# Kernel optimization log

Hardware: AMD Instinct MI355X
Metric: run time of the kernel (lower is better)

The kernel has to match this reference:

```python
import jax, jax.numpy as jnp
import numpy as np

WS = 14          # window size
NH = 12          # num heads
C = 768          # hidden dim
HD = C // NH     # head dim = 64
MLP = 3072       # mlp dim
EPS = 1e-6


def _layernorm(x, g, b):
    mu = jnp.mean(x, axis=-1, keepdims=True)
    var = jnp.mean(jnp.square(x - mu), axis=-1, keepdims=True)
    return (x - mu) * jax.lax.rsqrt(var + EPS) * g + b


def setup_inputs() -> dict:
    key = jax.random.key(0)
    ks = jax.random.split(key, 8)
    B, H, W = 8, 64, 64
    f32 = jnp.float32
    d = {}
    d["x"] = jax.random.normal(ks[0], (B, H, W, C), f32)
    d["ln1_g"] = jnp.ones((C,), f32)
    d["ln1_b"] = jnp.zeros((C,), f32)
    d["qkv_w"] = (jax.random.normal(ks[1], (C, 3 * C), f32) * 0.02)
    d["qkv_b"] = jnp.zeros((3 * C,), f32)
    d["proj_w"] = (jax.random.normal(ks[2], (C, C), f32) * 0.02)
    d["proj_b"] = jnp.zeros((C,), f32)
    d["rel_pos_h"] = (jax.random.normal(ks[3], (2 * WS - 1, HD), f32) * 0.02)
    d["rel_pos_w"] = (jax.random.normal(ks[4], (2 * WS - 1, HD), f32) * 0.02)
    d["ln2_g"] = jnp.ones((C,), f32)
    d["ln2_b"] = jnp.zeros((C,), f32)
    d["mlp_w1"] = (jax.random.normal(ks[5], (C, MLP), f32) * 0.02)
    d["mlp_b1"] = jnp.zeros((MLP,), f32)
    d["mlp_w2"] = (jax.random.normal(ks[6], (MLP, C), f32) * 0.02)
    d["mlp_b2"] = jnp.zeros((C,), f32)
    return d


def reference(x, ln1_g, ln1_b, qkv_w, qkv_b, proj_w, proj_b,
              rel_pos_h, rel_pos_w, ln2_g, ln2_b,
              mlp_w1, mlp_b1, mlp_w2, mlp_b2):
    B, H, W, _ = x.shape
    xn = _layernorm(x, ln1_g, ln1_b)

    # ---- window partition (pad to multiple of WS) ----
    pad_h = (-H) % WS
    pad_w = (-W) % WS
    Hp, Wp = H + pad_h, W + pad_w
    xp = jnp.pad(xn, ((0, 0), (0, pad_h), (0, pad_w), (0, 0)))
    # [B, Hp/WS, WS, Wp/WS, WS, C] -> [Bn, WS, WS, C]
    win = xp.reshape(B, Hp // WS, WS, Wp // WS, WS, C)
    win = win.transpose(0, 1, 3, 2, 4, 5).reshape(-1, WS, WS, C)
    Bn = win.shape[0]
    N = WS * WS

    # ---- attention with decomposed relative position bias ----
    qkv = win.reshape(Bn, N, C) @ qkv_w + qkv_b                 # [Bn, N, 3C]
    qkv = qkv.reshape(Bn, N, 3, NH, HD).transpose(2, 0, 3, 1, 4)
    qkv = qkv.reshape(3, Bn * NH, N, HD)
    q, k, v = qkv[0], qkv[1], qkv[2]

    scale = HD ** -0.5
    attn = jnp.einsum('bnd,bmd->bnm', q * scale, k)             # [Bn*NH, N, N]

    # rel coords: q_size == k_size == WS, rel_pos already has 2*WS-1 rows
    coords = jnp.arange(WS)[:, None] - jnp.arange(WS)[None, :] + (WS - 1)
    Rh = rel_pos_h[coords]                                      # [WS, WS, HD]
    Rw = rel_pos_w[coords]                                      # [WS, WS, HD]
    rq = q.reshape(Bn * NH, WS, WS, HD)
    rel_h = jnp.einsum('bhwc,hkc->bhwk', rq, Rh)                # [B', WS, WS, WS]
    rel_w = jnp.einsum('bhwc,wkc->bhwk', rq, Rw)
    attn = (attn.reshape(Bn * NH, WS, WS, WS, WS)
            + rel_h[:, :, :, :, None]
            + rel_w[:, :, :, None, :]).reshape(Bn * NH, N, N)

    attn = jax.nn.softmax(attn, axis=-1)
    out = jnp.einsum('bnm,bmd->bnd', attn, v)                   # [Bn*NH, N, HD]
    out = out.reshape(Bn, NH, WS, WS, HD).transpose(0, 2, 3, 1, 4).reshape(Bn, WS, WS, C)
    out = out @ proj_w + proj_b

    # ---- window unpartition ----
    out = out.reshape(B, Hp // WS, Wp // WS, WS, WS, C)
    out = out.transpose(0, 1, 3, 2, 4, 5).reshape(B, Hp, Wp, C)[:, :H, :W, :]

    x1 = x + out
    y = _layernorm(x1, ln2_g, ln2_b)
    y = jax.nn.gelu(y @ mlp_w1 + mlp_b1, approximate=False) @ mlp_w2 + mlp_b2
    return x1 + y
```

## Files before the change

### kernel.cpp

```cpp
#include <hip/hip_runtime.h>
#include <hip/hip_bf16.h>
#include <cstdint>
#include <cstddef>

using bf16 = __hip_bfloat16;
typedef __attribute__((ext_vector_type(8))) short short8;
typedef __attribute__((ext_vector_type(4))) float f32x4;

typedef __attribute__((address_space(1))) const void as1_void;
typedef __attribute__((address_space(3))) void as3_void;

__device__ __forceinline__ f32x4 mfma16x16x32(short8 a, short8 b, f32x4 c) {
  return __builtin_amdgcn_mfma_f32_16x16x32_bf16(a, b, c, 0, 0, 0);
}

__device__ __forceinline__ void gload_lds16(const void* g, void* l) {
  __builtin_amdgcn_global_load_lds((as1_void*)g, (as3_void*)l, 16, 0, 0);
}

__device__ __forceinline__ uint32_t cvtpk(float a, float b) {
  uint32_t r;
  asm("v_cvt_pk_bf16_f32 %0, %1, %2" : "=v"(r) : "v"(a), "v"(b));
  return r;
}

__device__ __forceinline__ float gelu_f(float v) {
  const float u = 0.7978845608f * v * (1.f + 0.044715f * v * v);
  const float e = __expf(-2.f * fabsf(u));
  const float t = (1.f - e) / (1.f + e);
  return 0.5f * v * (1.f + (u < 0.f ? -t : t));
}

static constexpr int MROWS = 39200;
static constexpr int MPAD  = 39424;
static constexpr int TOK2  = 32768;

__global__ __launch_bounds__(256)
void transpose_cast(const float* __restrict__ in, bf16* __restrict__ out, int K, int N) {
  __shared__ float t[32][33];
  const int tx = threadIdx.x & 31, ty = threadIdx.x >> 5;
  const int bx = blockIdx.x, by = blockIdx.y;
  const int x = bx * 32 + tx;
  for (int r = ty; r < 32; r += 8)
    t[r][tx] = in[(size_t)(by * 32 + r) * N + x];
  __syncthreads();
  const int xo = by * 32 + tx;
  for (int r = ty; r < 32; r += 8)
    out[(size_t)(bx * 32 + r) * K + xo] = __float2bfloat16(t[tx][r]);
}

__global__ __launch_bounds__(256)
void ln1_partition(const float* __restrict__ x, const float* __restrict__ g,
                   const float* __restrict__ bb, bf16* __restrict__ out) {
  const int token = blockIdx.x * 4 + (threadIdx.x >> 6);
  const int lane = threadIdx.x & 63;
  const int win = token / 196, tok = token % 196;
  const int b_ = win / 25, wh = (win / 5) % 5, ww = win % 5;
  const int i = tok / 14, j = tok % 14;
  const int h = wh * 14 + i, w = ww * 14 + j;
  bf16* o = out + (size_t)token * 768;
  if (h >= 64 || w >= 64) {
    for (int t = 0; t < 12; ++t) o[lane + 64 * t] = __float2bfloat16(0.f);
    return;
  }
  const float* src = x + ((size_t)((b_ * 64 + h) * 64 + w)) * 768;
  float vals[12], s = 0.f, ss = 0.f;
  #pragma unroll
  for (int t = 0; t < 12; ++t) {
    float v = src[lane + 64 * t];
    vals[t] = v; s += v; ss += v * v;
  }
  #pragma unroll
  for (int d = 32; d > 0; d >>= 1) { s += __shfl_xor(s, d); ss += __shfl_xor(ss, d); }
  const float mu = s * (1.f / 768.f);
  const float var = ss * (1.f / 768.f) - mu * mu;
  const float inv = rsqrtf(var + 1e-6f);
  #pragma unroll
  for (int t = 0; t < 12; ++t) {
    const int c = lane + 64 * t;
    o[c] = __float2bfloat16((vals[t] - mu) * inv * g[c] + bb[c]);
  }
}

__global__ __launch_bounds__(256)
void ln2_kernel(const float* __restrict__ x1, const float* __restrict__ g,
                const float* __restrict__ bb, bf16* __restrict__ out) {
  const int token = blockIdx.x * 4 + (threadIdx.x >> 6);
  const int lane = threadIdx.x & 63;
  const float* src = x1 + (size_t)token * 768;
  bf16* o = out + (size_t)token * 768;
  float vals[12], s = 0.f, ss = 0.f;
  #pragma unroll
  for (int t = 0; t < 12; ++t) {
    float v = src[lane + 64 * t];
    vals[t] = v; s += v; ss += v * v;
  }
  #pragma unroll
  for (int d = 32; d > 0; d >>= 1) { s += __shfl_xor(s, d); ss += __shfl_xor(ss, d); }
  const float mu = s * (1.f / 768.f);
  const float var = ss * (1.f / 768.f) - mu * mu;
  const float inv = rsqrtf(var + 1e-6f);
  #pragma unroll
  for (int t = 0; t < 12; ++t) {
    const int c = lane + 64 * t;
    o[c] = __float2bfloat16((vals[t] - mu) * inv * g[c] + bb[c]);
  }
}

template<int EPI>
__global__ __launch_bounds__(256)
void gemm_bf16(const bf16* __restrict__ A, const bf16* __restrict__ Bt,
               const float* __restrict__ bias, int K, int Mreal,
               const float* __restrict__ fin, float* __restrict__ fout,
               bf16* __restrict__ ob0, bf16* __restrict__ ob1, bf16* __restrict__ ob2) {
  __shared__ __align__(16) bf16 SMEM[16384];
  bf16* const lA0 = SMEM;
  bf16* const lA1 = SMEM + 4096;
  bf16* const lB0 = SMEM + 8192;
  bf16* const lB1 = SMEM + 12288;
  const int tid = threadIdx.x;
  const int lane = tid & 63, wv = tid >> 6;
  const int lr = lane & 15, hi = lane >> 4;
  const int wm = wv >> 1, wn = wv & 1;

  const int gx = gridDim.x;
  const int nwg = gx * gridDim.y;
  int lin = blockIdx.y * gx + blockIdx.x;
  {
    const int q8 = nwg >> 3, r8 = nwg & 7;
    const int xcd = lin & 7, pos = lin >> 3;
    lin = (xcd < r8 ? xcd * (q8 + 1) : r8 * (q8 + 1) + (xcd - r8) * q8) + pos;
  }
  const size_t arow0 = (size_t)(lin / gx) * 128;
  const size_t brow0 = (size_t)(lin % gx) * 128;
  f32x4 acc[4][4] = {};

  auto stage = [&](bf16* bufA, bf16* bufB, int kt) {
    const int k0 = kt * 32;
    #pragma unroll
    for (int it = 0; it < 2; ++it) {
      const int seg = it * 256 + tid;
      const int row = seg >> 2, kq = seg & 3;
      const size_t dst = (size_t)(it * 256 + wv * 64) * 8;
      if constexpr (EPI == 1) {
        const int k = k0 + kq * 8;
        gload_lds16(A + ((size_t)(k >> 6) * MPAD + arow0 + row) * 64 + (k & 63), bufA + dst);
      } else {
        gload_lds16(A + (arow0 + row) * K + k0 + kq * 8, bufA + dst);
      }
      gload_lds16(Bt + (brow0 + row) * K + k0 + kq * 8, bufB + dst);
    }
  };
  auto compute = [&](const bf16* bufA, const bf16* bufB) {
    short8 af[4], bfr[4];
    #pragma unroll
    for (int m = 0; m < 4; ++m) af[m] = *(const short8*)&bufA[(wm * 64 + m * 16 + lr) * 32 + hi * 8];
    #pragma unroll
    for (int n = 0; n < 4; ++n) bfr[n] = *(const short8*)&bufB[(wn * 64 + n * 16 + lr) * 32 + hi * 8];
    #pragma unroll
    for (int m = 0; m < 4; ++m)
      #pragma unroll
      for (int n = 0; n < 4; ++n)
        acc[m][n] = mfma16x16x32(af[m], bfr[n], acc[m][n]);
  };

  const int nt = K >> 5;
  stage(lA0, lB0, 0);
  __syncthreads();
  for (int t = 0; t < nt; t += 2) {
    if (t + 1 < nt) stage(lA1, lB1, t + 1);
    compute(lA0, lB0);
    __syncthreads();
    if (t + 2 < nt) stage(lA0, lB0, t + 2);
    compute(lA1, lB1);
    __syncthreads();
  }

  #pragma unroll
  for (int n = 0; n < 4; ++n) {
    const int col = (int)brow0 + wn * 64 + n * 16 + lr;
    const float bv = bias[col];
    #pragma unroll
    for (int m = 0; m < 4; ++m) {
      #pragma unroll
      for (int e = 0; e < 4; ++e) {
        const int row = (int)arow0 + wm * 64 + m * 16 + hi * 4 + e;
        const float v = acc[m][n][e] + bv;
        if (row < Mreal) {
          const int win = row / 196, tok = row % 196;
          const int b_ = win / 25, wh = (win / 5) % 5, ww = win % 5;
          const int i = tok / 14, j = tok % 14;
          const int h = wh * 14 + i, w = ww * 14 + j;
          if (h < 64 && w < 64) {
            const size_t idx = ((size_t)((b_ * 64 + h) * 64 + w)) * 768 + col;
            fout[idx] = fin[idx] + v;
          }
        }
      }
    }
  }
}

template<int MH, bool READB, int VMN>
__device__ __forceinline__ void gphase(
    const char* aR, const char* bR, int aoffB, int boffB,
    f32x4 (&acc)[8][4], short8& b0, short8& b1, short8& b2, short8& b3,
    const bf16* g0, const bf16* g1, char* sdst, int sdoff, int koff, bool doStage) {
  short8 a0 = *(const short8*)(aR + aoffB + (MH * 64 +  0) * 64);
  short8 a1 = *(const short8*)(aR + aoffB + (MH * 64 + 16) * 64);
  short8 a2 = *(const short8*)(aR + aoffB + (MH * 64 + 32) * 64);
  short8 a3 = *(const short8*)(aR + aoffB + (MH * 64 + 48) * 64);
  if constexpr (READB) {
    b0 = *(const short8*)(bR + boffB +  0 * 64);
    b1 = *(const short8*)(bR + boffB + 16 * 64);
    b2 = *(const short8*)(bR + boffB + 32 * 64);
    b3 = *(const short8*)(bR + boffB + 48 * 64);
  }
  if (doStage) {
    gload_lds16(g0 + koff, sdst + sdoff);
    gload_lds16(g1 + koff, sdst + sdoff + 8192);
  }
  __builtin_amdgcn_s_barrier();
  asm volatile("s_waitcnt lgkmcnt(0)" ::: "memory");
  __builtin_amdgcn_sched_barrier(0);
  __builtin_amdgcn_s_setprio(1);
  acc[MH*4+0][0] = mfma16x16x32(a0, b0, acc[MH*4+0][0]);
  acc[MH*4+0][1] = mfma16x16x32(a0, b1, acc[MH*4+0][1]);
  acc[MH*4+0][2] = mfma16x16x32(a0, b2, acc[MH*4+0][2]);
  acc[MH*4+0][3] = mfma16x16x32(a0, b3, acc[MH*4+0][3]);
  acc[MH*4+1][0] = mfma16x16x32(a1, b0, acc[MH*4+1][0]);
  acc[MH*4+1][1] = mfma16x16x32(a1, b1, acc[MH*4+1][1]);
  acc[MH*4+1][2] = mfma16x16x32(a1, b2, acc[MH*4+1][2]);
  acc[MH*4+1][3] = mfma16x16x32(a1, b3, acc[MH*4+1][3]);
  acc[MH*4+2][0] = mfma16x16x32(a2, b0, acc[MH*4+2][0]);
  acc[MH*4+2][1] = mfma16x16x32(a2, b1, acc[MH*4+2][1]);
  acc[MH*4+2][2] = mfma16x16x32(a2, b2, acc[MH*4+2][2]);
  acc[MH*4+2][3] = mfma16x16x32(a2, b3, acc[MH*4+2][3]);
  acc[MH*4+3][0] = mfma16x16x32(a3, b0, acc[MH*4+3][0]);
  acc[MH*4+3][1] = mfma16x16x32(a3, b1, acc[MH*4+3][1]);
  acc[MH*4+3][2] = mfma16x16x32(a3, b2, acc[MH*4+3][2]);
  acc[MH*4+3][3] = mfma16x16x32(a3, b3, acc[MH*4+3][3]);
  __builtin_amdgcn_s_setprio(0);
  if constexpr (VMN == 6) asm volatile("s_waitcnt vmcnt(6)" ::: "memory");
  if constexpr (VMN == 0) asm volatile("s_waitcnt vmcnt(0)" ::: "memory");
  __builtin_amdgcn_s_barrier();
}

template<int EPI, int KT>
__global__ __launch_bounds__(512)
void gemm256(const bf16* __restrict__ A, const bf16* __restrict__ Bt,
             const float* __restrict__ bias, int Mreal,
             const float* __restrict__ fin, float* __restrict__ fout,
             bf16* __restrict__ ob0, bf16* __restrict__ ob1, bf16* __restrict__ ob2) {
  __shared__ __align__(16) char SMEM[131072];
  char* const A0k0 = SMEM;
  char* const A0k1 = SMEM + 16384;
  char* const B0k0 = SMEM + 32768;
  char* const B0k1 = SMEM + 49152;
  char* const A1k0 = SMEM + 65536;
  char* const A1k1 = SMEM + 81920;
  char* const B1k0 = SMEM + 98304;
  char* const B1k1 = SMEM + 114688;
  const int tid = threadIdx.x;
  const int lane = tid & 63, wv = tid >> 6;
  const int lr = lane & 15, hi = lane >> 4;
  const int wm = wv >> 2, wn = wv & 3;

  const int gx = gridDim.x;
  const int nwg = gx * gridDim.y;
  int lin = blockIdx.y * gx + blockIdx.x;
  {
    const int q8 = nwg >> 3, r8 = nwg & 7;
    const int xcd = lin & 7, pos = lin >> 3;
    lin = (xcd < r8 ? xcd * (q8 + 1) : r8 * (q8 + 1) + (xcd - r8) * q8) + pos;
  }
  const size_t arow0 = (size_t)(lin / gx) * 256;
  const size_t brow0 = (size_t)(lin % gx) * 256;

  f32x4 acc[8][4] = {};
  short8 b0{}, b1{}, b2{}, b3{};
  constexpr int nt = KT >> 6;

  const int r0 = tid >> 2;
  const int c0 = (tid & 3) ^ ((r0 >> 1) & 3);
  const bf16* const gA0 = A  + (arow0 + r0) * (size_t)KT + c0 * 8;
  const bf16* const gA1 = gA0 + (size_t)128 * KT;
  const bf16* const gB0 = Bt + (brow0 + r0) * (size_t)KT + c0 * 8;
  const bf16* const gB1 = gB0 + (size_t)128 * KT;
  const int sdoff = tid << 4;
  const int cpos  = hi ^ ((lr >> 1) & 3);
  const int aoffB = (wm * 128 + lr) * 64 + (cpos << 4);
  const int boffB = (wn * 64 + lr) * 64 + (cpos << 4);

  auto stageU = [&](bool isB, int kt, int kh, char* dst) {
    if (kt >= nt) return;
    const int koff = (kt << 6) + (kh << 5);
    gload_lds16((isB ? gB0 : gA0) + koff, dst + sdoff);
    gload_lds16((isB ? gB1 : gA1) + koff, dst + sdoff + 8192);
  };

  stageU(true,  0, 0, B0k0);
  stageU(false, 0, 0, A0k0);
  stageU(true,  0, 1, B0k1);
  stageU(false, 0, 1, A0k1);
  stageU(true,  1, 0, B1k0);
  stageU(false, 1, 0, A1k0);
  stageU(true,  1, 1, B1k1);
  asm volatile("s_waitcnt vmcnt(6)" ::: "memory");
  __builtin_amdgcn_s_barrier();

  constexpr int niter = nt >> 1;
  for (int it = 0; it < niter - 1; ++it) {
    const int t = it * 2;
    const int kf1 = ((t+1) << 6) + 32, kf20 = (t+2) << 6, kf21 = kf20 + 32;
    const int kf30 = (t+3) << 6, kf31 = kf30 + 32;
    gphase<0,true ,-1>(A0k0, B0k0, aoffB, boffB, acc, b0,b1,b2,b3, gA0, gA1, A1k1, sdoff, kf1,  true);
    gphase<1,false,-1>(A0k0, B0k0, aoffB, boffB, acc, b0,b1,b2,b3, gB0, gB1, B0k0, sdoff, kf20, true);
    gphase<0,true ,-1>(A0k1, B0k1, aoffB, boffB, acc, b0,b1,b2,b3, gA0, gA1, A0k0, sdoff, kf20, true);
    gphase<1,false, 6>(A0k1, B0k1, aoffB, boffB, acc, b0,b1,b2,b3, gB0, gB1, B0k1, sdoff, kf21, true);
    gphase<0,true ,-1>(A1k0, B1k0, aoffB, boffB, acc, b0,b1,b2,b3, gA0, gA1, A0k1, sdoff, kf21, true);
    gphase<1,false,-1>(A1k0, B1k0, aoffB, boffB, acc, b0,b1,b2,b3, gB0, gB1, B1k0, sdoff, kf30, true);
    gphase<0,true ,-1>(A1k1, B1k1, aoffB, boffB, acc, b0,b1,b2,b3, gA0, gA1, A1k0, sdoff, kf30, true);
    gphase<1,false, 6>(A1k1, B1k1, aoffB, boffB, acc, b0,b1,b2,b3, gB0, gB1, B1k1, sdoff, kf31, true);
  }
  {
    const int t = nt - 2;
    const int kf1 = ((t+1) << 6) + 32;
    gphase<0,true ,-1>(A0k0, B0k0, aoffB, boffB, acc, b0,b1,b2,b3, gA0, gA1, A1k1, sdoff, kf1, true);
    gphase<1,false,-1>(A0k0, B0k0, aoffB, boffB, acc, b0,b1,b2,b3, gB0, gB1, B0k0, sdoff, 0, false);
    gphase<0,true ,-1>(A0k1, B0k1, aoffB, boffB, acc, b0,b1,b2,b3, gA0, gA1, A0k0, sdoff, 0, false);
    gphase<1,false, 0>(A0k1, B0k1, aoffB, boffB, acc, b0,b1,b2,b3, gB0, gB1, B0k1, sdoff, 0, false);
    gphase<0,true ,-1>(A1k0, B1k0, aoffB, boffB, acc, b0,b1,b2,b3, gA0, gA1, A0k1, sdoff, 0, false);
    gphase<1,false,-1>(A1k0, B1k0, aoffB, boffB, acc, b0,b1,b2,b3, gB0, gB1, B1k0, sdoff, 0, false);
    gphase<0,true ,-1>(A1k1, B1k1, aoffB, boffB, acc, b0,b1,b2,b3, gA0, gA1, A1k0, sdoff, 0, false);
    gphase<1,false, 0>(A1k1, B1k1, aoffB, boffB, acc, b0,b1,b2,b3, gB0, gB1, B1k1, sdoff, 0, false);
  }

  if constexpr (EPI == 0) {
    __syncthreads();
    char* ep = SMEM + wv * 16384;
    #pragma unroll
    for (int m = 0; m < 8; ++m) {
      #pragma unroll
      for (int n = 0; n < 4; ++n) {
        const int col = n * 16 + lr;
        const float bv = bias[(int)brow0 + wn * 64 + col];
        #pragma unroll
        for (int e = 0; e < 4; ++e) {
          const int row_l = m * 16 + hi * 4 + e;
          const int byte = row_l * 128 + col * 2;
          *(bf16*)(ep + (byte ^ ((row_l & 7) << 4))) = __float2bfloat16(acc[m][n][e] + bv);
        }
      }
    }
    __syncthreads();
    const int hchunk = ((int)brow0 + wn * 64) >> 6;
    const int which = hchunk / 12, head = hchunk % 12;
    bf16* dstb = (which == 0) ? ob0 : ((which == 1) ? ob1 : ob2);
    #pragma unroll
    for (int u = 0; u < 16; ++u) {
      const int unit = u * 64 + lane;
      const int row_l = unit >> 3, slot = unit & 7;
      const int byte = row_l * 128 + slot * 16;
      const short8 val = *(const short8*)(ep + (byte ^ ((row_l & 7) << 4)));
      const int grow = (int)arow0 + wm * 128 + row_l;
      if (grow < Mreal)
        *(short8*)&dstb[((size_t)head * MPAD + grow) * 64 + slot * 8] = val;
    }
  } else if constexpr (EPI == 2) {
    char* ep = SMEM + wv * 8192;
    #pragma unroll
    for (int h = 0; h < 2; ++h) {
      #pragma unroll
      for (int m2 = 0; m2 < 4; ++m2) {
        #pragma unroll
        for (int n = 0; n < 4; ++n) {
          const int col = n * 16 + lr;
          const float bv = bias[(int)brow0 + wn * 64 + col];
          #pragma unroll
          for (int e = 0; e < 4; ++e) {
            const int row_l = m2 * 16 + hi * 4 + e;
            const float v = gelu_f(acc[h * 4 + m2][n][e] + bv);
            *(bf16*)(ep + row_l * 128 + (((col >> 3) ^ (row_l & 7)) << 4) + ((col & 7) << 1))
                = __float2bfloat16(v);
          }
        }
      }
      #pragma unroll
      for (int p = 0; p < 8; ++p) {
        const int row_l = p * 8 + (lane >> 3);
        const int slot  = lane & 7;
        const short8 val = *(const short8*)(ep + row_l * 128 + ((slot ^ (row_l & 7)) << 4));
        const size_t grow = arow0 + wm * 128 + h * 64 + row_l;
        const int gcol = (int)brow0 + wn * 64 + slot * 8;
        *(short8*)&ob0[grow * 3072 + gcol] = val;
      }
    }
  } else {
    #pragma unroll
    for (int n = 0; n < 4; ++n) {
      const int col = (int)brow0 + wn * 64 + n * 16 + lr;
      const float bv = bias[col];
      #pragma unroll
      for (int m = 0; m < 8; ++m) {
        #pragma unroll
        for (int e = 0; e < 4; ++e) {
          const size_t row = arow0 + wm * 128 + m * 16 + hi * 4 + e;
          const size_t idx = row * 768 + col;
          fout[idx] = fin[idx] + acc[m][n][e] + bv;
        }
      }
    }
  }
}

__global__ __launch_bounds__(512, 2)
void attn_kernel(const bf16* __restrict__ qb, const bf16* __restrict__ kb,
                 const bf16* __restrict__ vb, const float* __restrict__ rph,
                 const float* __restrict__ rpw, bf16* __restrict__ aout) {
  __shared__ __align__(16) char SM[65248];
  bf16* pbh    = (bf16*)SM;
  bf16* pbw    = (bf16*)(SM + 4096);
  bf16* Gh     = (bf16*)(SM + 8192);
  bf16* Gw     = (bf16*)(SM + 23168);
  char* klds   = SM;
  char* vtb    = SM + 25600;
  bf16* relh_s = (bf16*)(SM + 54272);
  bf16* relw_s = (bf16*)(SM + 59760);

  const int bh = blockIdx.x;
  const int win = bh / 12, head = bh % 12;
  const size_t base = ((size_t)head * MPAD + win * 196) * 64;
  const bf16* Q  = qb + base;
  const bf16* Kp = kb + base;
  const bf16* Vp = vb + base;
  const int tid = threadIdx.x, lane = tid & 63, wv = tid >> 6;
  const int lr = lane & 15, hi = lane >> 4;

  for (int i = tid; i < 32 * 64; i += 512) {
    const int r = i >> 6, c = i & 63;
    const bool ok = r < 27;
    pbh[i] = __float2bfloat16(ok ? rph[r * 64 + c] : 0.f);
    pbw[i] = __float2bfloat16(ok ? rpw[r * 64 + c] : 0.f);
  }
  __syncthreads();
  {
    short8 bh00 = *(const short8*)&pbh[(lr) * 64 + hi * 8];
    short8 bh01 = *(const short8*)&pbh[(lr) * 64 + 32 + hi * 8];
    short8 bh10 = *(const short8*)&pbh[(16 + lr) * 64 + hi * 8];
    short8 bh11 = *(const short8*)&pbh[(16 + lr) * 64 + 32 + hi * 8];
    short8 bw00 = *(const short8*)&pbw[(lr) * 64 + hi * 8];
    short8 bw01 = *(const short8*)&pbw[(lr) * 64 + 32 + hi * 8];
    short8 bw10 = *(const short8*)&pbw[(16 + lr) * 64 + hi * 8];
    short8 bw11 = *(const short8*)&pbw[(16 + lr) * 64 + 32 + hi * 8];
    for (int mt = wv; mt < 13; mt += 8) {
      const short8 a0 = *(const short8*)&Q[(mt * 16 + lr) * 64 + hi * 8];
      const short8 a1 = *(const short8*)&Q[(mt * 16 + lr) * 64 + 32 + hi * 8];
      f32x4 g0 = {}, g1 = {}, g2 = {}, g3 = {};
      g0 = mfma16x16x32(a0, bh00, g0); g0 = mfma16x16x32(a1, bh01, g0);
      g1 = mfma16x16x32(a0, bh10, g1); g1 = mfma16x16x32(a1, bh11, g1);
      g2 = mfma16x16x32(a0, bw00, g2); g2 = mfma16x16x32(a1, bw01, g2);
      g3 = mfma16x16x32(a0, bw10, g3); g3 = mfma16x16x32(a1, bw11, g3);
      #pragma unroll
      for (int e = 0; e < 4; ++e) {
        const int row = mt * 16 + hi * 4 + e;
        Gh[row * 36 + lr]      = __float2bfloat16(g0[e]);
        Gh[row * 36 + 16 + lr] = __float2bfloat16(g1[e]);
        Gw[row * 36 + lr]      = __float2bfloat16(g2[e]);
        Gw[row * 36 + 16 + lr] = __float2bfloat16(g3[e]);
      }
    }
  }
  __syncthreads();
  bf16 ghr[6], gwr[6];
  #pragma unroll
  for (int t = 0; t < 6; ++t) {
    const int i = tid + t * 512;
    if (i < 196 * 14) {
      const int q = i / 14, kk = i - (i / 14) * 14;
      const int rh = q / 14 - kk + 13;
      const int rw2 = q - (q / 14) * 14 - kk + 13;
      ghr[t] = Gh[q * 36 + rh];
      gwr[t] = Gw[q * 36 + rw2];
    }
  }
  __syncthreads();
  #pragma unroll
  for (int t = 0; t < 6; ++t) {
    const int i = tid + t * 512;
    if (i < 196 * 14) { relh_s[i] = ghr[t]; relw_s[i] = gwr[t]; }
  }
  for (int c = wv; c < 25; c += 8) {
    const int row = c * 8 + (lane >> 3);
    const int ch  = (lane & 7) ^ (row & 7);
    gload_lds16(Kp + row * 64 + ch * 8, klds + c * 1024);
  }
  for (int i = tid; i < 196 * 8; i += 512) {
    const int key = i >> 3, dg = (i & 7) * 8;
    const short8 v = *(const short8*)&Vp[key * 64 + dg];
    #pragma unroll
    for (int j = 0; j < 8; ++j) {
      const int idx = (dg + j) * 448 + key * 2;
      *(bf16*)(vtb + (idx ^ (j << 4))) = ((const bf16*)&v)[j];
    }
  }
  for (int i = tid; i < 64 * 28; i += 512) {
    const int d = i / 28, key = 196 + i - (i / 28) * 28;
    const int idx = d * 448 + key * 2;
    *(bf16*)(vtb + (idx ^ ((d & 7) << 4))) = __float2bfloat16(0.f);
  }
  __syncthreads();

  for (int qt = wv; qt < 13; qt += 8) {
    const int q = qt * 16 + lr;
    const int qc = q < 196 ? q : 195;
    const short8 bq0 = *(const short8*)&Q[(qt * 16 + lr) * 64 + hi * 8];
    const short8 bq1 = *(const short8*)&Q[(qt * 16 + lr) * 64 + 32 + hi * 8];
    f32x4 s[13];
    __builtin_amdgcn_s_setprio(1);
    #pragma unroll
    for (int nt = 0; nt < 13; ++nt) {
      const int key = nt * 16 + lr;
      const char* kr = klds + key * 128;
      const short8 ka0 = *(const short8*)(kr + (((hi) ^ (key & 7)) << 4));
      const short8 ka1 = *(const short8*)(kr + (((hi + 4) ^ (key & 7)) << 4));
      f32x4 z = {};
      z = mfma16x16x32(ka0, bq0, z);
      z = mfma16x16x32(ka1, bq1, z);
      s[nt] = z;
    }
    __builtin_amdgcn_s_setprio(0);
    float mx = -3.0e38f;
    #pragma unroll
    for (int nt = 0; nt < 13; ++nt) {
      #pragma unroll
      for (int e = 0; e < 4; ++e) {
        const int key = nt * 16 + hi * 4 + e;
        const int kh = key / 14, kw = key - kh * 14;
        float v = s[nt][e] * 0.125f + __bfloat162float(relh_s[qc * 14 + kh])
                                    + __bfloat162float(relw_s[qc * 14 + kw]);
        v = (key < 196) ? v : -3.0e38f;
        s[nt][e] = v;
        mx = fmaxf(mx, v);
      }
    }
    mx = fmaxf(mx, __shfl_xor(mx, 16));
    mx = fmaxf(mx, __shfl_xor(mx, 32));
    float sm = 0.f;
    uint32_t pk0[14], pk1[14];
    #pragma unroll
    for (int nt = 0; nt < 13; ++nt) {
      const float p0 = __expf(s[nt][0] - mx);
      const float p1 = __expf(s[nt][1] - mx);
      const float p2 = __expf(s[nt][2] - mx);
      const float p3 = __expf(s[nt][3] - mx);
      sm += (p0 + p1) + (p2 + p3);
      pk0[nt] = cvtpk(p0, p1);
      pk1[nt] = cvtpk(p2, p3);
    }
    pk0[13] = 0u; pk1[13] = 0u;
    sm += __shfl_xor(sm, 16);
    sm += __shfl_xor(sm, 32);
    const float rinv = 1.f / sm;
    f32x4 o[4] = {};
    #pragma unroll
    for (int kk = 0; kk < 7; ++kk) {
      const uint32_t x0 = pk0[2 * kk],     x1 = pk1[2 * kk];
      const uint32_t y0 = pk0[2 * kk + 1], y1 = pk1[2 * kk + 1];
      const uint32_t s0 = (hi < 2) ? y0 : x0, s1 = (hi < 2) ? y1 : x1;
      const uint32_t t0 = __shfl_xor(s0, 32), t1 = __shfl_xor(s1, 32);
      const uint32_t o0 = (hi < 2) ? x0 : y0, o1 = (hi < 2) ? x1 : y1;
      const bool sendOwn = (hi == 1) || (hi == 2);
      const uint32_t u0 = sendOwn ? o0 : t0, u1 = sendOwn ? o1 : t1;
      const uint32_t r0 = __shfl_xor(u0, 16), r1 = __shfl_xor(u1, 16);
      union { uint32_t u[4]; short8 v; } pf;
      pf.u[0] = (hi == 0) ? x0 : ((hi == 2) ? t0 : r0);
      pf.u[1] = (hi == 0) ? x1 : ((hi == 2) ? t1 : r1);
      pf.u[2] = (hi == 3) ? y0 : ((hi == 1) ? t0 : r0);
      pf.u[3] = (hi == 3) ? y1 : ((hi == 1) ? t1 : r1);
      __builtin_amdgcn_s_setprio(1);
      #pragma unroll
      for (int n2 = 0; n2 < 4; ++n2) {
        const int d = n2 * 16 + lr;
        const int idx = d * 448 + (kk * 32 + hi * 8) * 2;
        const short8 va = *(const short8*)(vtb + (idx ^ ((lr & 7) << 4)));
        o[n2] = mfma16x16x32(va, pf.v, o[n2]);
      }
      __builtin_amdgcn_s_setprio(0);
    }
    if (q < 196) {
      bf16* orow = aout + ((size_t)head * MPAD + win * 196 + q) * 64;
      #pragma unroll
      for (int n2 = 0; n2 < 4; ++n2) {
        uint32_t d0 = cvtpk(o[n2][0] * rinv, o[n2][1] * rinv);
        uint32_t d1 = cvtpk(o[n2][2] * rinv, o[n2][3] * rinv);
        uint32_t* dst = (uint32_t*)&orow[n2 * 16 + hi * 4];
        dst[0] = d0; dst[1] = d1;
      }
    }
  }
}

extern "C" void kernel_launch(void* const* d_in, const int* in_sizes, int n_in,
                              void* d_out, int out_size, void* d_ws, size_t ws_size,
                              hipStream_t stream) {
  (void)in_sizes; (void)n_in; (void)out_size; (void)ws_size;
  const float* x      = (const float*)d_in[0];
  const float* ln1_g  = (const float*)d_in[1];
  const float* ln1_b  = (const float*)d_in[2];
  const float* qkv_w  = (const float*)d_in[3];
  const float* qkv_b  = (const float*)d_in[4];
  const float* proj_w = (const float*)d_in[5];
  const float* proj_b = (const float*)d_in[6];
  const float* rph    = (const float*)d_in[7];
  const float* rpw    = (const float*)d_in[8];
  const float* ln2_g  = (const float*)d_in[9];
  const float* ln2_b  = (const float*)d_in[10];
  const float* w1     = (const float*)d_in[11];
  const float* b1v    = (const float*)d_in[12];
  const float* w2     = (const float*)d_in[13];
  const float* b2v    = (const float*)d_in[14];
  float* outp = (float*)d_out;

  char* ws = (char*)d_ws;
  size_t off = 0;
  auto alloc = [&](size_t bytes) { char* p = ws + off; off += (bytes + 255) & ~(size_t)255; return p; };
  bf16* qkv_wt  = (bf16*)alloc((size_t)2304 * 768 * 2);
  bf16* proj_wt = (bf16*)alloc((size_t)768 * 768 * 2);
  bf16* w1t     = (bf16*)alloc((size_t)3072 * 768 * 2);
  bf16* w2t     = (bf16*)alloc((size_t)768 * 3072 * 2);
  const size_t szB1 = (size_t)MPAD * 768 * 2;
  const size_t szB2 = (size_t)TOK2 * 768 * 2;
  char* regB = alloc(szB1 > szB2 ? szB1 : szB2);
  const size_t szQKV = (size_t)3 * 12 * MPAD * 64 * 2;
  const size_t szH   = (size_t)TOK2 * 3072 * 2;
  char* regC = alloc(szQKV > szH ? szQKV : szH);

  bf16* xnwin   = (bf16*)regB;
  bf16* attnout = (bf16*)regB;
  bf16* xn2     = (bf16*)regB;
  bf16* qbuf    = (bf16*)regC;
  bf16* kbuf    = qbuf + (size_t)12 * MPAD * 64;
  bf16* vbuf    = kbuf + (size_t)12 * MPAD * 64;
  bf16* hbuf    = (bf16*)regC;

  transpose_cast<<<dim3(2304 / 32, 768 / 32), 256, 0, stream>>>(qkv_w, qkv_wt, 768, 2304);
  transpose_cast<<<dim3(768 / 32, 768 / 32), 256, 0, stream>>>(proj_w, proj_wt, 768, 768);
  transpose_cast<<<dim3(3072 / 32, 768 / 32), 256, 0, stream>>>(w1, w1t, 768, 3072);
  transpose_cast<<<dim3(768 / 32, 3072 / 32), 256, 0, stream>>>(w2, w2t, 3072, 768);

  ln1_partition<<<dim3(MROWS / 4), 256, 0, stream>>>(x, ln1_g, ln1_b, xnwin);

  gemm256<0, 768><<<dim3(2304 / 256, MPAD / 256), 512, 0, stream>>>(
      xnwin, qkv_wt, qkv_b, MROWS, nullptr, nullptr, qbuf, kbuf, vbuf);

  attn_kernel<<<dim3(2400), 512, 0, stream>>>(qbuf, kbuf, vbuf, rph, rpw, attnout);

  gemm_bf16<1><<<dim3(768 / 128, MPAD / 128), 256, 0, stream>>>(
      attnout, proj_wt, proj_b, 768, MROWS, x, outp, nullptr, nullptr, nullptr);

  ln2_kernel<<<dim3(TOK2 / 4), 256, 0, stream>>>(outp, ln2_g, ln2_b, xn2);

  gemm256<2, 768><<<dim3(3072 / 256, TOK2 / 256), 512, 0, stream>>>(
      xn2, w1t, b1v, TOK2, nullptr, nullptr, hbuf, nullptr, nullptr);
  gemm256<3, 3072><<<dim3(768 / 256, TOK2 / 256), 512, 0, stream>>>(
      hbuf, w2t, b2v, TOK2, outp, outp, nullptr, nullptr, nullptr);
}
```

Before: 1.042 ms.

## Shrink GEMM LDS pipeline to two-stage double buffer and split epilogue

Replaces the four-slot (two k-tiles by two k-halves) LDS staging in the 256x256 GEMM with a simple two-buffer ping-pong over 32-wide k steps. Each phase now waits for all outstanding loads before its barrier, so less memory latency is hidden. The QKV epilogue is also reworked to write through per-wave 8KB LDS tiles in two halves instead of 16KB tiles, which removes the extra syncthreads. LDS use halves to 64KB, which may permit more co-resident workgroups, at the cost of a shallower prefetch depth.

```diff
diff --git a/kernel.cpp b/kernel.cpp
--- a/kernel.cpp
+++ b/kernel.cpp
@@ -241,7 +241,6 @@
   acc[MH*4+3][2] = mfma16x16x32(a3, b2, acc[MH*4+3][2]);
   acc[MH*4+3][3] = mfma16x16x32(a3, b3, acc[MH*4+3][3]);
   __builtin_amdgcn_s_setprio(0);
-  if constexpr (VMN == 6) asm volatile("s_waitcnt vmcnt(6)" ::: "memory");
   if constexpr (VMN == 0) asm volatile("s_waitcnt vmcnt(0)" ::: "memory");
   __builtin_amdgcn_s_barrier();
 }
@@ -252,15 +251,11 @@
              const float* __restrict__ bias, int Mreal,
              const float* __restrict__ fin, float* __restrict__ fout,
              bf16* __restrict__ ob0, bf16* __restrict__ ob1, bf16* __restrict__ ob2) {
-  __shared__ __align__(16) char SMEM[131072];
-  char* const A0k0 = SMEM;
-  char* const A0k1 = SMEM + 16384;
-  char* const B0k0 = SMEM + 32768;
-  char* const B0k1 = SMEM + 49152;
-  char* const A1k0 = SMEM + 65536;
-  char* const A1k1 = SMEM + 81920;
-  char* const B1k0 = SMEM + 98304;
-  char* const B1k1 = SMEM + 114688;
+  __shared__ __align__(16) char SMEM[65536];
+  char* const A0 = SMEM;
+  char* const B0 = SMEM + 16384;
+  char* const A1 = SMEM + 32768;
+  char* const B1 = SMEM + 49152;
   const int tid = threadIdx.x;
   const int lane = tid & 63, wv = tid >> 6;
   const int lr = lane & 15, hi = lane >> 4;
@@ -279,7 +274,7 @@
 
   f32x4 acc[8][4] = {};
   short8 b0{}, b1{}, b2{}, b3{};
-  constexpr int nt = KT >> 6;
+  constexpr int nt = KT >> 5;
 
   const int r0 = tid >> 2;
   const int c0 = (tid & 3) ^ ((r0 >> 1) & 3);
@@ -292,80 +287,52 @@
   const int aoffB = (wm * 128 + lr) * 64 + (cpos << 4);
   const int boffB = (wn * 64 + lr) * 64 + (cpos << 4);
 
-  auto stageU = [&](bool isB, int kt, int kh, char* dst) {
-    if (kt >= nt) return;
-    const int koff = (kt << 6) + (kh << 5);
-    gload_lds16((isB ? gB0 : gA0) + koff, dst + sdoff);
-    gload_lds16((isB ? gB1 : gA1) + koff, dst + sdoff + 8192);
-  };
-
-  stageU(true,  0, 0, B0k0);
-  stageU(false, 0, 0, A0k0);
-  stageU(true,  0, 1, B0k1);
-  stageU(false, 0, 1, A0k1);
-  stageU(true,  1, 0, B1k0);
-  stageU(false, 1, 0, A1k0);
-  stageU(true,  1, 1, B1k1);
-  asm volatile("s_waitcnt vmcnt(6)" ::: "memory");
+  gload_lds16(gA0, A0 + sdoff);
+  gload_lds16(gA1, A0 + sdoff + 8192);
+  gload_lds16(gB0, B0 + sdoff);
+  gload_lds16(gB1, B0 + sdoff + 8192);
+  asm volatile("s_waitcnt vmcnt(0)" ::: "memory");
   __builtin_amdgcn_s_barrier();
 
-  constexpr int niter = nt >> 1;
-  for (int it = 0; it < niter - 1; ++it) {
-    const int t = it * 2;
-    const int kf1 = ((t+1) << 6) + 32, kf20 = (t+2) << 6, kf21 = kf20 + 32;
-    const int kf30 = (t+3) << 6, kf31 = kf30 + 32;
-    gphase<0,true ,-1>(A0k0, B0k0, aoffB, boffB, acc, b0,b1,b2,b3, gA0, gA1, A1k1, sdoff, kf1,  true);
-    gphase<1,false,-1>(A0k0, B0k0, aoffB, boffB, acc, b0,b1,b2,b3, gB0, gB1, B0k0, sdoff, kf20, true);
-    gphase<0,true ,-1>(A0k1, B0k1, aoffB, boffB, acc, b0,b1,b2,b3, gA0, gA1, A0k0, sdoff, kf20, true);
-    gphase<1,false, 6>(A0k1, B0k1, aoffB, boffB, acc, b0,b1,b2,b3, gB0, gB1, B0k1, sdoff, kf21, true);
-    gphase<0,true ,-1>(A1k0, B1k0, aoffB, boffB, acc, b0,b1,b2,b3, gA0, gA1, A0k1, sdoff, kf21, true);
-    gphase<1,false,-1>(A1k0, B1k0, aoffB, boffB, acc, b0,b1,b2,b3, gB0, gB1, B1k0, sdoff, kf30, true);
-    gphase<0,true ,-1>(A1k1, B1k1, aoffB, boffB, acc, b0,b1,b2,b3, gA0, gA1, A1k0, sdoff, kf30, true);
-    gphase<1,false, 6>(A1k1, B1k1, aoffB, boffB, acc, b0,b1,b2,b3, gB0, gB1, B1k1, sdoff, kf31, true);
-  }
-  {
-    const int t = nt - 2;
-    const int kf1 = ((t+1) << 6) + 32;
-    gphase<0,true ,-1>(A0k0, B0k0, aoffB, boffB, acc, b0,b1,b2,b3, gA0, gA1, A1k1, sdoff, kf1, true);
-    gphase<1,false,-1>(A0k0, B0k0, aoffB, boffB, acc, b0,b1,b2,b3, gB0, gB1, B0k0, sdoff, 0, false);
-    gphase<0,true ,-1>(A0k1, B0k1, aoffB, boffB, acc, b0,b1,b2,b3, gA0, gA1, A0k0, sdoff, 0, false);
-    gphase<1,false, 0>(A0k1, B0k1, aoffB, boffB, acc, b0,b1,b2,b3, gB0, gB1, B0k1, sdoff, 0, false);
-    gphase<0,true ,-1>(A1k0, B1k0, aoffB, boffB, acc, b0,b1,b2,b3, gA0, gA1, A0k1, sdoff, 0, false);
-    gphase<1,false,-1>(A1k0, B1k0, aoffB, boffB, acc, b0,b1,b2,b3, gB0, gB1, B1k0, sdoff, 0, false);
-    gphase<0,true ,-1>(A1k1, B1k1, aoffB, boffB, acc, b0,b1,b2,b3, gA0, gA1, A1k0, sdoff, 0, false);
-    gphase<1,false, 0>(A1k1, B1k1, aoffB, boffB, acc, b0,b1,b2,b3, gB0, gB1, B1k1, sdoff, 0, false);
+  for (int t = 0; t < nt; t += 2) {
+    const int k1 = (t + 1) << 5, k2 = (t + 2) << 5;
+    const bool s1 = (t + 1) < nt, s2 = (t + 2) < nt;
+    gphase<0,true ,-1>(A0, B0, aoffB, boffB, acc, b0,b1,b2,b3, gA0, gA1, A1, sdoff, k1, s1);
+    gphase<1,false, 0>(A0, B0, aoffB, boffB, acc, b0,b1,b2,b3, gB0, gB1, B1, sdoff, k1, s1);
+    gphase<0,true ,-1>(A1, B1, aoffB, boffB, acc, b0,b1,b2,b3, gA0, gA1, A0, sdoff, k2, s2);
+    gphase<1,false, 0>(A1, B1, aoffB, boffB, acc, b0,b1,b2,b3, gB0, gB1, B0, sdoff, k2, s2);
   }
 
   if constexpr (EPI == 0) {
-    __syncthreads();
-    char* ep = SMEM + wv * 16384;
-    #pragma unroll
-    for (int m = 0; m < 8; ++m) {
-      #pragma unroll
-      for (int n = 0; n < 4; ++n) {
-        const int col = n * 16 + lr;
-        const float bv = bias[(int)brow0 + wn * 64 + col];
-        #pragma unroll
-        for (int e = 0; e < 4; ++e) {
-          const int row_l = m * 16 + hi * 4 + e;
-          const int byte = row_l * 128 + col * 2;
-          *(bf16*)(ep + (byte ^ ((row_l & 7) << 4))) = __float2bfloat16(acc[m][n][e] + bv);
-        }
-      }
-    }
-    __syncthreads();
+    char* ep = SMEM + wv * 8192;
     const int hchunk = ((int)brow0 + wn * 64) >> 6;
     const int which = hchunk / 12, head = hchunk % 12;
     bf16* dstb = (which == 0) ? ob0 : ((which == 1) ? ob1 : ob2);
     #pragma unroll
-    for (int u = 0; u < 16; ++u) {
-      const int unit = u * 64 + lane;
-      const int row_l = unit >> 3, slot = unit & 7;
-      const int byte = row_l * 128 + slot * 16;
-      const short8 val = *(const short8*)(ep + (byte ^ ((row_l & 7) << 4)));
-      const int grow = (int)arow0 + wm * 128 + row_l;
-      if (grow < Mreal)
-        *(short8*)&dstb[((size_t)head * MPAD + grow) * 64 + slot * 8] = val;
+    for (int h = 0; h < 2; ++h) {
+      #pragma unroll
+      for (int m2 = 0; m2 < 4; ++m2) {
+        #pragma unroll
+        for (int n = 0; n < 4; ++n) {
+          const int col = n * 16 + lr;
+          const float bv = bias[(int)brow0 + wn * 64 + col];
+          #pragma unroll
+          for (int e = 0; e < 4; ++e) {
+            const int row_l = m2 * 16 + hi * 4 + e;
+            *(bf16*)(ep + row_l * 128 + (((col >> 3) ^ (row_l & 7)) << 4) + ((col & 7) << 1))
+                = __float2bfloat16(acc[h * 4 + m2][n][e] + bv);
+          }
+        }
+      }
+      #pragma unroll
+      for (int p = 0; p < 8; ++p) {
+        const int row_l = p * 8 + (lane >> 3);
+        const int slot  = lane & 7;
+        const short8 val = *(const short8*)(ep + row_l * 128 + ((slot ^ (row_l & 7)) << 4));
+        const int grow = (int)arow0 + wm * 128 + h * 64 + row_l;
+        if (grow < Mreal)
+          *(short8*)&dstb[((size_t)head * MPAD + grow) * 64 + slot * 8] = val;
+      }
     }
   } else if constexpr (EPI == 2) {
     char* ep = SMEM + wv * 8192;
```

Measured after the change: 1.068 ms. 2.5% more time.

## Run projection GEMM on the 256x256 pipelined kernel with head-major A

Applied to the files above, without the earlier changes.

Replaces the simple 128x128 double-buffered projection GEMM with the 256x256 pipelined gemm256 kernel. A new template flag handles the head-major A layout produced by attention, by striding K over heads. A new epilogue adds the residual and unpartitions windows. This aims for higher MFMA utilisation and better operand reuse, at the cost of fewer, larger blocks, which can waste part of a wave on this N=768 shape.

```diff
diff --git a/kernel.cpp b/kernel.cpp
--- a/kernel.cpp
+++ b/kernel.cpp
@@ -104,100 +104,6 @@
   for (int t = 0; t < 12; ++t) {
     const int c = lane + 64 * t;
     o[c] = __float2bfloat16((vals[t] - mu) * inv * g[c] + bb[c]);
-  }
-}
-
-template<int EPI>
-__global__ __launch_bounds__(256)
-void gemm_bf16(const bf16* __restrict__ A, const bf16* __restrict__ Bt,
-               const float* __restrict__ bias, int K, int Mreal,
-               const float* __restrict__ fin, float* __restrict__ fout,
-               bf16* __restrict__ ob0, bf16* __restrict__ ob1, bf16* __restrict__ ob2) {
-  __shared__ __align__(16) bf16 SMEM[16384];
-  bf16* const lA0 = SMEM;
-  bf16* const lA1 = SMEM + 4096;
-  bf16* const lB0 = SMEM + 8192;
-  bf16* const lB1 = SMEM + 12288;
-  const int tid = threadIdx.x;
-  const int lane = tid & 63, wv = tid >> 6;
-  const int lr = lane & 15, hi = lane >> 4;
-  const int wm = wv >> 1, wn = wv & 1;
-
-  const int gx = gridDim.x;
-  const int nwg = gx * gridDim.y;
-  int lin = blockIdx.y * gx + blockIdx.x;
-  {
-    const int q8 = nwg >> 3, r8 = nwg & 7;
-    const int xcd = lin & 7, pos = lin >> 3;
-    lin = (xcd < r8 ? xcd * (q8 + 1) : r8 * (q8 + 1) + (xcd - r8) * q8) + pos;
-  }
-  const size_t arow0 = (size_t)(lin / gx) * 128;
-  const size_t brow0 = (size_t)(lin % gx) * 128;
-  f32x4 acc[4][4] = {};
-
-  auto stage = [&](bf16* bufA, bf16* bufB, int kt) {
-    const int k0 = kt * 32;
-    #pragma unroll
-    for (int it = 0; it < 2; ++it) {
-      const int seg = it * 256 + tid;
-      const int row = seg >> 2, kq = seg & 3;
-      const size_t dst = (size_t)(it * 256 + wv * 64) * 8;
-      if constexpr (EPI == 1) {
-        const int k = k0 + kq * 8;
-        gload_lds16(A + ((size_t)(k >> 6) * MPAD + arow0 + row) * 64 + (k & 63), bufA + dst);
-      } else {
-        gload_lds16(A + (arow0 + row) * K + k0 + kq * 8, bufA + dst);
-      }
-      gload_lds16(Bt + (brow0 + row) * K + k0 + kq * 8, bufB + dst);
-    }
-  };
-  auto compute = [&](const bf16* bufA, const bf16* bufB) {
-    short8 af[4], bfr[4];
-    #pragma unroll
-    for (int m = 0; m < 4; ++m) af[m] = *(const short8*)&bufA[(wm * 64 + m * 16 + lr) * 32 + hi * 8];
-    #pragma unroll
-    for (int n = 0; n < 4; ++n) bfr[n] = *(const short8*)&bufB[(wn * 64 + n * 16 + lr) * 32 + hi * 8];
-    #pragma unroll
-    for (int m = 0; m < 4; ++m)
-      #pragma unroll
-      for (int n = 0; n < 4; ++n)
-        acc[m][n] = mfma16x16x32(af[m], bfr[n], acc[m][n]);
-  };
-
-  const int nt = K >> 5;
-  stage(lA0, lB0, 0);
-  __syncthreads();
-  for (int t = 0; t < nt; t += 2) {
-    if (t + 1 < nt) stage(lA1, lB1, t + 1);
-    compute(lA0, lB0);
-    __syncthreads();
-    if (t + 2 < nt) stage(lA0, lB0, t + 2);
-    compute(lA1, lB1);
-    __syncthreads();
-  }
-
-  #pragma unroll
-  for (int n = 0; n < 4; ++n) {
-    const int col = (int)brow0 + wn * 64 + n * 16 + lr;
-    const float bv = bias[col];
-    #pragma unroll
-    for (int m = 0; m < 4; ++m) {
-      #pragma unroll
-      for (int e = 0; e < 4; ++e) {
-        const int row = (int)arow0 + wm * 64 + m * 16 + hi * 4 + e;
-        const float v = acc[m][n][e] + bv;
-        if (row < Mreal) {
-          const int win = row / 196, tok = row % 196;
-          const int b_ = win / 25, wh = (win / 5) % 5, ww = win % 5;
-          const int i = tok / 14, j = tok % 14;
-          const int h = wh * 14 + i, w = ww * 14 + j;
-          if (h < 64 && w < 64) {
-            const size_t idx = ((size_t)((b_ * 64 + h) * 64 + w)) * 768 + col;
-            fout[idx] = fin[idx] + v;
-          }
-        }
-      }
-    }
   }
 }
 
@@ -246,7 +152,7 @@
   __builtin_amdgcn_s_barrier();
 }
 
-template<int EPI, int KT>
+template<int EPI, int KT, bool AHEAD>
 __global__ __launch_bounds__(512)
 void gemm256(const bf16* __restrict__ A, const bf16* __restrict__ Bt,
              const float* __restrict__ bias, int Mreal,
@@ -280,11 +186,13 @@
   f32x4 acc[8][4] = {};
   short8 b0{}, b1{}, b2{}, b3{};
   constexpr int nt = KT >> 6;
+  constexpr int ASTRIDE = AHEAD ? (MPAD * 64) : 64;
 
   const int r0 = tid >> 2;
   const int c0 = (tid & 3) ^ ((r0 >> 1) & 3);
-  const bf16* const gA0 = A  + (arow0 + r0) * (size_t)KT + c0 * 8;
-  const bf16* const gA1 = gA0 + (size_t)128 * KT;
+  const bf16* const gA0 = AHEAD ? (A + (arow0 + r0) * 64 + c0 * 8)
+                                : (A + (arow0 + r0) * (size_t)KT + c0 * 8);
+  const bf16* const gA1 = gA0 + (size_t)128 * (AHEAD ? 64 : KT);
   const bf16* const gB0 = Bt + (brow0 + r0) * (size_t)KT + c0 * 8;
   const bf16* const gB1 = gB0 + (size_t)128 * KT;
   const int sdoff = tid << 4;
@@ -294,7 +202,7 @@
 
   auto stageU = [&](bool isB, int kt, int kh, char* dst) {
     if (kt >= nt) return;
-    const int koff = (kt << 6) + (kh << 5);
+    const int koff = isB ? ((kt << 6) + (kh << 5)) : (kt * ASTRIDE + kh * 32);
     gload_lds16((isB ? gB0 : gA0) + koff, dst + sdoff);
     gload_lds16((isB ? gB1 : gA1) + koff, dst + sdoff + 8192);
   };
@@ -312,21 +220,24 @@
   constexpr int niter = nt >> 1;
   for (int it = 0; it < niter - 1; ++it) {
     const int t = it * 2;
-    const int kf1 = ((t+1) << 6) + 32, kf20 = (t+2) << 6, kf21 = kf20 + 32;
-    const int kf30 = (t+3) << 6, kf31 = kf30 + 32;
-    gphase<0,true ,-1>(A0k0, B0k0, aoffB, boffB, acc, b0,b1,b2,b3, gA0, gA1, A1k1, sdoff, kf1,  true);
-    gphase<1,false,-1>(A0k0, B0k0, aoffB, boffB, acc, b0,b1,b2,b3, gB0, gB1, B0k0, sdoff, kf20, true);
-    gphase<0,true ,-1>(A0k1, B0k1, aoffB, boffB, acc, b0,b1,b2,b3, gA0, gA1, A0k0, sdoff, kf20, true);
-    gphase<1,false, 6>(A0k1, B0k1, aoffB, boffB, acc, b0,b1,b2,b3, gB0, gB1, B0k1, sdoff, kf21, true);
-    gphase<0,true ,-1>(A1k0, B1k0, aoffB, boffB, acc, b0,b1,b2,b3, gA0, gA1, A0k1, sdoff, kf21, true);
-    gphase<1,false,-1>(A1k0, B1k0, aoffB, boffB, acc, b0,b1,b2,b3, gB0, gB1, B1k0, sdoff, kf30, true);
-    gphase<0,true ,-1>(A1k1, B1k1, aoffB, boffB, acc, b0,b1,b2,b3, gA0, gA1, A1k0, sdoff, kf30, true);
-    gphase<1,false, 6>(A1k1, B1k1, aoffB, boffB, acc, b0,b1,b2,b3, gB0, gB1, B1k1, sdoff, kf31, true);
+    const int kfa1  = (t + 1) * ASTRIDE + 32;
+    const int kfa20 = (t + 2) * ASTRIDE, kfa21 = kfa20 + 32;
+    const int kfa30 = (t + 3) * ASTRIDE;
+    const int kfb20 = (t + 2) << 6, kfb21 = kfb20 + 32;
+    const int kfb30 = (t + 3) << 6, kfb31 = kfb30 + 32;
+    gphase<0,true ,-1>(A0k0, B0k0, aoffB, boffB, acc, b0,b1,b2,b3, gA0, gA1, A1k1, sdoff, kfa1,  true);
+    gphase<1,false,-1>(A0k0, B0k0, aoffB, boffB, acc, b0,b1,b2,b3, gB0, gB1, B0k0, sdoff, kfb20, true);
+    gphase<0,true ,-1>(A0k1, B0k1, aoffB, boffB, acc, b0,b1,b2,b3, gA0, gA1, A0k0, sdoff, kfa20, true);
+    gphase<1,false, 6>(A0k1, B0k1, aoffB, boffB, acc, b0,b1,b2,b3, gB0, gB1, B0k1, sdoff, kfb21, true);
+    gphase<0,true ,-1>(A1k0, B1k0, aoffB, boffB, acc, b0,b1,b2,b3, gA0, gA1, A0k1, sdoff, kfa21, true);
+    gphase<1,false,-1>(A1k0, B1k0, aoffB, boffB, acc, b0,b1,b2,b3, gB0, gB1, B1k0, sdoff, kfb30, true);
+    gphase<0,true ,-1>(A1k1, B1k1, aoffB, boffB, acc, b0,b1,b2,b3, gA0, gA1, A1k0, sdoff, kfa30, true);
+    gphase<1,false, 6>(A1k1, B1k1, aoffB, boffB, acc, b0,b1,b2,b3, gB0, gB1, B1k1, sdoff, kfb31, true);
   }
   {
     const int t = nt - 2;
-    const int kf1 = ((t+1) << 6) + 32;
-    gphase<0,true ,-1>(A0k0, B0k0, aoffB, boffB, acc, b0,b1,b2,b3, gA0, gA1, A1k1, sdoff, kf1, true);
+    const int kfa1 = (t + 1) * ASTRIDE + 32;
+    gphase<0,true ,-1>(A0k0, B0k0, aoffB, boffB, acc, b0,b1,b2,b3, gA0, gA1, A1k1, sdoff, kfa1, true);
     gphase<1,false,-1>(A0k0, B0k0, aoffB, boffB, acc, b0,b1,b2,b3, gB0, gB1, B0k0, sdoff, 0, false);
     gphase<0,true ,-1>(A0k1, B0k1, aoffB, boffB, acc, b0,b1,b2,b3, gA0, gA1, A0k0, sdoff, 0, false);
     gphase<1,false, 0>(A0k1, B0k1, aoffB, boffB, acc, b0,b1,b2,b3, gB0, gB1, B0k1, sdoff, 0, false);
@@ -366,6 +277,30 @@
       const int grow = (int)arow0 + wm * 128 + row_l;
       if (grow < Mreal)
         *(short8*)&dstb[((size_t)head * MPAD + grow) * 64 + slot * 8] = val;
+    }
+  } else if constexpr (EPI == 1) {
+    #pragma unroll
+    for (int n = 0; n < 4; ++n) {
+      const int col = (int)brow0 + wn * 64 + n * 16 + lr;
+      const float bv = bias[col];
+      #pragma unroll
+      for (int m = 0; m < 8; ++m) {
+        #pragma unroll
+        for (int e = 0; e < 4; ++e) {
+          const int row = (int)arow0 + wm * 128 + m * 16 + hi * 4 + e;
+          const float v = acc[m][n][e] + bv;
+          if (row < Mreal) {
+            const int win = row / 196, tok = row % 196;
+            const int b_ = win / 25, wh = (win / 5) % 5, ww = win % 5;
+            const int i = tok / 14, j = tok % 14;
+            const int h = wh * 14 + i, w = ww * 14 + j;
+            if (h < 64 && w < 64) {
+              const size_t idx = ((size_t)((b_ * 64 + h) * 64 + w)) * 768 + col;
+              fout[idx] = fin[idx] + v;
+            }
+          }
+        }
+      }
     }
   } else if constexpr (EPI == 2) {
     char* ep = SMEM + wv * 8192;
@@ -651,18 +586,18 @@
 
   ln1_partition<<<dim3(MROWS / 4), 256, 0, stream>>>(x, ln1_g, ln1_b, xnwin);
 
-  gemm256<0, 768><<<dim3(2304 / 256, MPAD / 256), 512, 0, stream>>>(
+  gemm256<0, 768, false><<<dim3(2304 / 256, MPAD / 256), 512, 0, stream>>>(
       xnwin, qkv_wt, qkv_b, MROWS, nullptr, nullptr, qbuf, kbuf, vbuf);
 
   attn_kernel<<<dim3(2400), 512, 0, stream>>>(qbuf, kbuf, vbuf, rph, rpw, attnout);
 
-  gemm_bf16<1><<<dim3(768 / 128, MPAD / 128), 256, 0, stream>>>(
-      attnout, proj_wt, proj_b, 768, MROWS, x, outp, nullptr, nullptr, nullptr);
+  gemm256<1, 768, true><<<dim3(768 / 256, MPAD / 256), 512, 0, stream>>>(
+      attnout, proj_wt, proj_b, MROWS, x, outp, nullptr, nullptr, nullptr);
 
   ln2_kernel<<<dim3(TOK2 / 4), 256, 0, stream>>>(outp, ln2_g, ln2_b, xn2);
 
-  gemm256<2, 768><<<dim3(3072 / 256, TOK2 / 256), 512, 0, stream>>>(
+  gemm256<2, 768, false><<<dim3(3072 / 256, TOK2 / 256), 512, 0, stream>>>(
       xn2, w1t, b1v, TOK2, nullptr, nullptr, hbuf, nullptr, nullptr);
-  gemm256<3, 3072><<<dim3(768 / 256, TOK2 / 256), 512, 0, stream>>>(
+  gemm256<3, 3072, false><<<dim3(768 / 256, TOK2 / 256), 512, 0, stream>>>(
       hbuf, w2t, b2v, TOK2, outp, outp, nullptr, nullptr, nullptr);
 }
```

New measurement: 1.059 ms. No clear change (+1.6%).
